# Optimization experiments

Measured on AMD Instinct MI355X. Metric: run time of the kernel, lower is better.

The kernel has to match this reference:

```python
import jax, jax.numpy as jnp
import numpy as np

N, C, B = 65536, 512, 4
H, P = 8, 256           # num_heads, patch_size
D = C // H              # head_dim = 64


def setup_inputs() -> dict:
    key = jax.random.key(0)
    k0, k1, k2 = jax.random.split(key, 3)
    x = jax.random.normal(k0, (N, C), dtype=jnp.float32)
    # sorted batch ids, equal-sized scenes (each divisible by patch_size)
    batch = (jnp.arange(N) // (N // B)).astype(jnp.int32)
    w_qkv = jax.random.normal(k1, (C, 3 * C), dtype=jnp.float32) * (C ** -0.5)
    b_qkv = jnp.zeros((3 * C,), dtype=jnp.float32)
    w_proj = jax.random.normal(k2, (C, C), dtype=jnp.float32) * (C ** -0.5)
    b_proj = jnp.zeros((C,), dtype=jnp.float32)
    return {"x": x, "batch": batch, "w_qkv": w_qkv, "b_qkv": b_qkv,
            "w_proj": w_proj, "b_proj": b_proj}


def reference(x, batch, w_qkv, b_qkv, w_proj, b_proj):
    # batch is sorted with per-scene counts divisible by P, so the original
    # per-batch mask/pad loop is exactly a global reshape into patches.
    n = x.shape[0]
    scale = D ** -0.5
    qkv = (x @ w_qkv + b_qkv).reshape(n, 3, H, D)
    q, k, v = qkv[:, 0], qkv[:, 1], qkv[:, 2]          # (N, H, D)
    q = q.reshape(-1, P, H, D)                          # (nP, P, H, D)
    k = k.reshape(-1, P, H, D)
    v = v.reshape(-1, P, H, D)
    attn = jnp.einsum('pihd,pjhd->phij', q, k) * scale  # (nP, H, P, P)
    attn = jax.nn.softmax(attn, axis=-1)
    out = jnp.einsum('phij,pjhd->pihd', attn, v)        # (nP, P, H, D)
    out = out.reshape(n, C)
    return out @ w_proj + b_proj
```

## Files before the change

### kernel.cpp

```cpp
#include <hip/hip_runtime.h>
#include <hip/hip_bf16.h>
#include <cstdint>

typedef __attribute__((ext_vector_type(8))) short bf16x8;
typedef __attribute__((ext_vector_type(4))) float f32x4;
typedef unsigned short u16;
typedef unsigned int u32;

#define MFMA16(a, b, c) __builtin_amdgcn_mfma_f32_16x16x32_bf16(a, b, c, 0, 0, 0)

__device__ __forceinline__ u16 f2bf(float f) {
  u32 u = __builtin_bit_cast(u32, f);
  u32 r = (u + 0x7fffu + ((u >> 16) & 1u)) >> 16;
  return (u16)r;
}

__device__ __forceinline__ void gload_lds16(const u16* g, u16* l) {
#if __has_builtin(__builtin_amdgcn_global_load_lds)
  __builtin_amdgcn_global_load_lds(
      (const __attribute__((address_space(1))) u32*)(const void*)g,
      (__attribute__((address_space(3))) u32*)(void*)l, 16, 0, 0);
#else
  *(uint4*)l = *(const uint4*)g;
#endif
}


__global__ __launch_bounds__(256) void cvt_x_kernel(const float* __restrict__ in,
                                                    u16* __restrict__ out, int n4) {
  const int stride = gridDim.x * blockDim.x;
  for (int i = blockIdx.x * blockDim.x + threadIdx.x; i < n4; i += stride) {
    float4 v = ((const float4*)in)[i];
    ushort4 o;
    o.x = f2bf(v.x); o.y = f2bf(v.y); o.z = f2bf(v.z); o.w = f2bf(v.w);
    ((ushort4*)out)[i] = o;
  }
}

__global__ __launch_bounds__(256) void transpose_kernel(const float* __restrict__ in,
                                                        u16* __restrict__ out,
                                                        int rows, int cols) {
  int idx = blockIdx.x * 256 + threadIdx.x;
  if (idx < rows * cols) {
    int c = idx / rows, r = idx - c * rows;
    out[idx] = f2bf(in[(size_t)r * cols + c]);
  }
}


template <bool OUT_BF16>
__global__ __launch_bounds__(256) void gemm_bt(const u16* __restrict__ A,
                                               const u16* __restrict__ Bt,
                                               const float* __restrict__ bias,
                                               void* __restrict__ Cout, int Ncols) {
  constexpr int K = 512;
  const int tm = blockIdx.x, tn = blockIdx.y;
  const int t = threadIdx.x;
  const int lane = t & 63, w = t >> 6;
  const int wr = w >> 1, wc = w & 1;
  const int fr = lane & 15, fq = lane >> 4;

  __shared__ __align__(16) u16 Als[128 * 64];
  __shared__ __align__(16) u16 Bls[128 * 64];

  f32x4 acc[4][4] = {};

  const u16* Ab = A + (size_t)tm * 128 * K;
  const u16* Bb = Bt + (size_t)tn * 128 * K;
  const int srow = t >> 3;
  const int scol = (t & 7) * 8;

  for (int ks = 0; ks < K; ks += 64) {
#pragma unroll
    for (int c = 0; c < 4; ++c) {
      gload_lds16(Ab + (size_t)(c * 32 + srow) * K + ks + scol, Als + c * 2048 + t * 8);
      gload_lds16(Bb + (size_t)(c * 32 + srow) * K + ks + scol, Bls + c * 2048 + t * 8);
    }
    __syncthreads();
#pragma unroll
    for (int kk = 0; kk < 2; ++kk) {
      bf16x8 af[4], bfr[4];
#pragma unroll
      for (int mt = 0; mt < 4; ++mt)
        af[mt] = *(const bf16x8*)(Als + (wr * 64 + mt * 16 + fr) * 64 + kk * 32 + fq * 8);
#pragma unroll
      for (int nt = 0; nt < 4; ++nt)
        bfr[nt] = *(const bf16x8*)(Bls + (wc * 64 + nt * 16 + fr) * 64 + kk * 32 + fq * 8);
#pragma unroll
      for (int mt = 0; mt < 4; ++mt)
#pragma unroll
        for (int nt = 0; nt < 4; ++nt)
          acc[mt][nt] = MFMA16(af[mt], bfr[nt], acc[mt][nt]);
    }
    __syncthreads();
  }

#pragma unroll
  for (int nt = 0; nt < 4; ++nt) {
    const int col = tn * 128 + wc * 64 + nt * 16 + fr;
    const float bv = bias[col];
#pragma unroll
    for (int mt = 0; mt < 4; ++mt) {
#pragma unroll
      for (int r = 0; r < 4; ++r) {
        const int row = tm * 128 + wr * 64 + mt * 16 + fq * 4 + r;
        float v = acc[mt][nt][r] + bv;
        if (OUT_BF16)
          ((u16*)Cout)[(size_t)row * Ncols + col] = f2bf(v);
        else
          ((float*)Cout)[(size_t)row * Ncols + col] = v;
      }
    }
  }
}


__global__ __launch_bounds__(512) void attn_kernel(const u16* __restrict__ qkv,
                                                   u16* __restrict__ out) {
  const int p = blockIdx.x, h = blockIdx.y;
  const int t = threadIdx.x, lane = t & 63, w = t >> 6;
  const int fr = lane & 15, fq = lane >> 4;

  __shared__ __align__(16) u16 Kls[256][72];
  __shared__ __align__(16) u16 Vt[64][264];
  __shared__ __align__(16) u16 Pls[8][32][72];

  const u16* base = qkv + (size_t)p * 256 * 1536 + h * 64;

#pragma unroll
  for (int it = 0; it < 4; ++it) {
    int chunk = it * 512 + t;
    int row = chunk >> 3, c8 = (chunk & 7) * 8;
    *(uint4*)&Kls[row][c8] = *(const uint4*)(base + (size_t)row * 1536 + 512 + c8);
  }
  {
    int token = t & 255, dh = (t >> 8) * 32;
    const u16* vs = base + (size_t)token * 1536 + 1024 + dh;
    uint4 b0 = *(const uint4*)(vs);
    uint4 b1 = *(const uint4*)(vs + 8);
    uint4 b2 = *(const uint4*)(vs + 16);
    uint4 b3 = *(const uint4*)(vs + 24);
    u16 tmp[32];
    *(uint4*)&tmp[0] = b0; *(uint4*)&tmp[8] = b1;
    *(uint4*)&tmp[16] = b2; *(uint4*)&tmp[24] = b3;
#pragma unroll
    for (int dd = 0; dd < 32; ++dd) Vt[dh + dd][token] = tmp[dd];
  }
  bf16x8 qf[2][2];
#pragma unroll
  for (int mt = 0; mt < 2; ++mt)
#pragma unroll
    for (int kk = 0; kk < 2; ++kk)
      qf[mt][kk] = *(const bf16x8*)(base + (size_t)(w * 32 + mt * 16 + fr) * 1536 + kk * 32 + fq * 8);
  __syncthreads();

  f32x4 Oc[2][4] = {};
  float mrow[2][4], lrow[2][4];
#pragma unroll
  for (int mt = 0; mt < 2; ++mt)
#pragma unroll
    for (int r = 0; r < 4; ++r) { mrow[mt][r] = -1e30f; lrow[mt][r] = 0.f; }

  for (int jb = 0; jb < 4; ++jb) {
    f32x4 S[2][4] = {};
#pragma unroll
    for (int kk = 0; kk < 2; ++kk) {
      bf16x8 kb[4];
#pragma unroll
      for (int jt = 0; jt < 4; ++jt)
        kb[jt] = *(const bf16x8*)&Kls[jb * 64 + jt * 16 + fr][kk * 32 + fq * 8];
#pragma unroll
      for (int mt = 0; mt < 2; ++mt)
#pragma unroll
        for (int jt = 0; jt < 4; ++jt)
          S[mt][jt] = MFMA16(qf[mt][kk], kb[jt], S[mt][jt]);
    }
#pragma unroll
    for (int mt = 0; mt < 2; ++mt) {
#pragma unroll
      for (int r = 0; r < 4; ++r) {
        float s0 = S[mt][0][r] * 0.125f, s1 = S[mt][1][r] * 0.125f;
        float s2 = S[mt][2][r] * 0.125f, s3 = S[mt][3][r] * 0.125f;
        float mx = fmaxf(fmaxf(s0, s1), fmaxf(s2, s3));
#pragma unroll
        for (int d = 1; d < 16; d <<= 1) mx = fmaxf(mx, __shfl_xor(mx, d, 64));
        float mnew = fmaxf(mrow[mt][r], mx);
        float alpha = __expf(mrow[mt][r] - mnew);
        mrow[mt][r] = mnew;
        float e0 = __expf(s0 - mnew), e1 = __expf(s1 - mnew);
        float e2 = __expf(s2 - mnew), e3 = __expf(s3 - mnew);
        S[mt][0][r] = e0; S[mt][1][r] = e1; S[mt][2][r] = e2; S[mt][3][r] = e3;
        float rs = e0 + e1 + e2 + e3;
#pragma unroll
        for (int d = 1; d < 16; d <<= 1) rs += __shfl_xor(rs, d, 64);
        lrow[mt][r] = lrow[mt][r] * alpha + rs;
#pragma unroll
        for (int dt = 0; dt < 4; ++dt) Oc[mt][dt][r] *= alpha;
      }
    }
#pragma unroll
    for (int mt = 0; mt < 2; ++mt)
#pragma unroll
      for (int jt = 0; jt < 4; ++jt)
#pragma unroll
        for (int r = 0; r < 4; ++r)
          Pls[w][mt * 16 + fq * 4 + r][jt * 16 + fr] = f2bf(S[mt][jt][r]);
    __syncthreads();
#pragma unroll
    for (int kk = 0; kk < 2; ++kk) {
      bf16x8 pa[2], vb[4];
#pragma unroll
      for (int mt = 0; mt < 2; ++mt)
        pa[mt] = *(const bf16x8*)&Pls[w][mt * 16 + fr][kk * 32 + fq * 8];
#pragma unroll
      for (int dt = 0; dt < 4; ++dt)
        vb[dt] = *(const bf16x8*)&Vt[dt * 16 + fr][jb * 64 + kk * 32 + fq * 8];
#pragma unroll
      for (int mt = 0; mt < 2; ++mt)
#pragma unroll
        for (int dt = 0; dt < 4; ++dt)
          Oc[mt][dt] = MFMA16(pa[mt], vb[dt], Oc[mt][dt]);
    }
  }
#pragma unroll
  for (int mt = 0; mt < 2; ++mt) {
#pragma unroll
    for (int r = 0; r < 4; ++r) {
      const float inv = 1.0f / lrow[mt][r];
      const int token = p * 256 + w * 32 + mt * 16 + fq * 4 + r;
#pragma unroll
      for (int dt = 0; dt < 4; ++dt)
        out[(size_t)token * 512 + h * 64 + dt * 16 + fr] = f2bf(Oc[mt][dt][r] * inv);
    }
  }
}


extern "C" void kernel_launch(void* const* d_in, const int* in_sizes, int n_in,
                              void* d_out, int out_size, void* d_ws, size_t ws_size,
                              hipStream_t stream) {
  const float* x      = (const float*)d_in[0];
  const float* w_qkv  = (const float*)d_in[2];
  const float* b_qkv  = (const float*)d_in[3];
  const float* w_proj = (const float*)d_in[4];
  const float* b_proj = (const float*)d_in[5];

  char* ws = (char*)d_ws;
  u16* xa     = (u16*)ws;
  u16* wqkvT  = (u16*)(ws + 67108864);
  u16* wprojT = (u16*)(ws + 68681728);
  u16* qkv    = (u16*)(ws + 69206016);
  u16* attn   = xa;

  cvt_x_kernel<<<2048, 256, 0, stream>>>(x, xa, 65536 * 512 / 4);
  transpose_kernel<<<(512 * 1536 + 255) / 256, 256, 0, stream>>>(w_qkv, wqkvT, 512, 1536);
  transpose_kernel<<<(512 * 512 + 255) / 256, 256, 0, stream>>>(w_proj, wprojT, 512, 512);

  gemm_bt<true><<<dim3(512, 12), 256, 0, stream>>>(xa, wqkvT, b_qkv, qkv, 1536);
  attn_kernel<<<dim3(256, 8), 512, 0, stream>>>(qkv, attn);
  gemm_bt<false><<<dim3(512, 4), 256, 0, stream>>>(attn, wprojT, b_proj, d_out, 512);
}
```

Baseline: 637.1 us.

## Replace GEMMs with 256x256-tile, 8-wave, double-buffered pipelined kernel

Both projection GEMMs now use a 256x256 tile per workgroup with 8 waves and double-buffered LDS. Global-to-LDS loads are interleaved with MFMA phases under explicit waitcnt and barrier control. LDS reads use an XOR swizzle to avoid bank conflicts, the workgroup order is remapped for better L2 locality, and MFMA phases raise wave priority. The aim is to hide memory latency and raise data reuse and MFMA utilisation, at the cost of higher register and LDS pressure and a fragile hand-written schedule.

```diff
diff --git a/kernel.cpp b/kernel.cpp
--- a/kernel.cpp
+++ b/kernel.cpp
@@ -16,13 +16,9 @@
 }
 
 __device__ __forceinline__ void gload_lds16(const u16* g, u16* l) {
-#if __has_builtin(__builtin_amdgcn_global_load_lds)
   __builtin_amdgcn_global_load_lds(
       (const __attribute__((address_space(1))) u32*)(const void*)g,
       (__attribute__((address_space(3))) u32*)(void*)l, 16, 0, 0);
-#else
-  *(uint4*)l = *(const uint4*)g;
-#endif
 }
 
 
@@ -48,62 +44,122 @@
 }
 
 
-template <bool OUT_BF16>
-__global__ __launch_bounds__(256) void gemm_bt(const u16* __restrict__ A,
-                                               const u16* __restrict__ Bt,
-                                               const float* __restrict__ bias,
-                                               void* __restrict__ Cout, int Ncols) {
+template <bool OUT_BF16, int NTN>
+__global__ __launch_bounds__(512, 2) void gemm8(const u16* __restrict__ A,
+                                                const u16* __restrict__ Bt,
+                                                const float* __restrict__ bias,
+                                                void* __restrict__ Cout, int Ncols) {
   constexpr int K = 512;
-  const int tm = blockIdx.x, tn = blockIdx.y;
-  const int t = threadIdx.x;
-  const int lane = t & 63, w = t >> 6;
-  const int wr = w >> 1, wc = w & 1;
+  const int nwg = gridDim.x;
+  const int q8 = nwg >> 3;
+  const int L = (blockIdx.x & 7) * q8 + (blockIdx.x >> 3);
+  const int tm = L / NTN, tn = L % NTN;
+
+  const int t = threadIdx.x, lane = t & 63, w = t >> 6;
+  const int wr = w >> 2, wc = w & 3;
   const int fr = lane & 15, fq = lane >> 4;
 
-  __shared__ __align__(16) u16 Als[128 * 64];
-  __shared__ __align__(16) u16 Bls[128 * 64];
-
-  f32x4 acc[4][4] = {};
-
-  const u16* Ab = A + (size_t)tm * 128 * K;
-  const u16* Bb = Bt + (size_t)tn * 128 * K;
-  const int srow = t >> 3;
-  const int scol = (t & 7) * 8;
-
-  for (int ks = 0; ks < K; ks += 64) {
-#pragma unroll
-    for (int c = 0; c < 4; ++c) {
-      gload_lds16(Ab + (size_t)(c * 32 + srow) * K + ks + scol, Als + c * 2048 + t * 8);
-      gload_lds16(Bb + (size_t)(c * 32 + srow) * K + ks + scol, Bls + c * 2048 + t * 8);
-    }
-    __syncthreads();
-#pragma unroll
-    for (int kk = 0; kk < 2; ++kk) {
-      bf16x8 af[4], bfr[4];
-#pragma unroll
-      for (int mt = 0; mt < 4; ++mt)
-        af[mt] = *(const bf16x8*)(Als + (wr * 64 + mt * 16 + fr) * 64 + kk * 32 + fq * 8);
-#pragma unroll
-      for (int nt = 0; nt < 4; ++nt)
-        bfr[nt] = *(const bf16x8*)(Bls + (wc * 64 + nt * 16 + fr) * 64 + kk * 32 + fq * 8);
-#pragma unroll
-      for (int mt = 0; mt < 4; ++mt)
-#pragma unroll
-        for (int nt = 0; nt < 4; ++nt)
-          acc[mt][nt] = MFMA16(af[mt], bfr[nt], acc[mt][nt]);
-    }
-    __syncthreads();
-  }
+  __shared__ __align__(16) u16 lds[2][2][2][8192];
+
+  const u16* Ab = A + (size_t)tm * 256 * K;
+  const u16* Bb = Bt + (size_t)tn * 256 * K;
+
+  int srow[2], scol[2];
+#pragma unroll
+  for (int i = 0; i < 2; ++i) {
+    const int cidx = t + i * 512;
+    const int rr = cidx >> 7, cc = (cidx >> 6) & 1, r16 = (cidx >> 2) & 15, qq = cidx & 3;
+    const int c8 = qq ^ ((r16 >> 3) << 1);
+    srow[i] = rr * 16 + r16;
+    scol[i] = cc * 32 + c8 * 8;
+  }
+
+  f32x4 acc[8][4] = {};
+  bf16x8 areg[4][2];
+  bf16x8 breg[4][2];
+
+  const int swz = (fq * 16) ^ ((fr & 8) << 2);
+
+#define STAGE(SB, SOP, SH, STK)                                                  \
+  {                                                                              \
+    const u16* gb_ = (SOP == 0) ? Ab : Bb;                                       \
+    u16* lb_ = &lds[SB][SOP][SH][0];                                             \
+    _Pragma("unroll") for (int i_ = 0; i_ < 2; ++i_) {                           \
+      gload_lds16(gb_ + (size_t)(SH * 128 + srow[i_]) * K + (STK) * 64 + scol[i_],\
+                  lb_ + (t + i_ * 512) * 8);                                     \
+    }                                                                            \
+  }
+
+#define LDA(RB, MH)                                                              \
+  {                                                                              \
+    const char* ab_ = (const char*)&lds[RB][0][wr][0];                           \
+    _Pragma("unroll") for (int m_ = 0; m_ < 4; ++m_)                             \
+      _Pragma("unroll") for (int kk_ = 0; kk_ < 2; ++kk_)                        \
+        areg[m_][kk_] = *(const bf16x8*)(ab_ + ((MH) * 4 + m_) * 2048 +          \
+                                         kk_ * 1024 + fr * 64 + swz);            \
+  }
+
+#define LDB(RB, NH)                                                              \
+  {                                                                              \
+    const char* bb_ = (const char*)&lds[RB][1][wc >> 1][0];                      \
+    _Pragma("unroll") for (int n_ = 0; n_ < 2; ++n_)                             \
+      _Pragma("unroll") for (int kk_ = 0; kk_ < 2; ++kk_)                        \
+        breg[(NH) * 2 + n_][kk_] = *(const bf16x8*)(bb_ +                        \
+            ((wc & 1) * 4 + (NH) * 2 + n_) * 2048 + kk_ * 1024 + fr * 64 + swz); \
+  }
+
+#define MMA(MH, NH)                                                              \
+  {                                                                              \
+    __builtin_amdgcn_s_setprio(1);                                               \
+    _Pragma("unroll") for (int m_ = 0; m_ < 4; ++m_)                             \
+      _Pragma("unroll") for (int n_ = 0; n_ < 2; ++n_)                           \
+        _Pragma("unroll") for (int kk_ = 0; kk_ < 2; ++kk_)                      \
+          acc[(MH) * 4 + m_][(NH) * 2 + n_] =                                    \
+              MFMA16(areg[m_][kk_], breg[(NH) * 2 + n_][kk_],                    \
+                     acc[(MH) * 4 + m_][(NH) * 2 + n_]);                         \
+    __builtin_amdgcn_s_setprio(0);                                               \
+  }
+
+#define BAR() __builtin_amdgcn_s_barrier()
+#define WLGKM() asm volatile("s_waitcnt lgkmcnt(0)" ::: "memory")
+#define WV4() asm volatile("s_waitcnt vmcnt(4)" ::: "memory")
+#define WV0() asm volatile("s_waitcnt vmcnt(0)" ::: "memory")
+
+  STAGE(0, 1, 0, 0) STAGE(0, 1, 1, 0) STAGE(0, 0, 0, 0) STAGE(0, 0, 1, 0)
+  STAGE(1, 1, 0, 1) STAGE(1, 1, 1, 1)
+  WV4();
+  BAR();
+
+#pragma unroll 1
+  for (int s = 0; s < 3; ++s) {
+    const int o1 = 2 * s + 1, e2 = 2 * s + 2, o3 = 2 * s + 3;
+    LDA(0, 0) LDB(0, 0) STAGE(1, 0, 0, o1) BAR(); WLGKM(); MMA(0, 0) BAR();
+    LDB(0, 1) STAGE(1, 0, 1, o1) BAR(); WLGKM(); MMA(0, 1) BAR();
+    LDA(0, 1) STAGE(0, 1, 0, e2) BAR(); WLGKM(); MMA(1, 0) BAR();
+    STAGE(0, 1, 1, e2) BAR(); MMA(1, 1) WV4(); BAR();
+    LDA(1, 0) LDB(1, 0) STAGE(0, 0, 0, e2) BAR(); WLGKM(); MMA(0, 0) BAR();
+    LDB(1, 1) STAGE(0, 0, 1, e2) BAR(); WLGKM(); MMA(0, 1) BAR();
+    LDA(1, 1) STAGE(1, 1, 0, o3) BAR(); WLGKM(); MMA(1, 0) BAR();
+    STAGE(1, 1, 1, o3) BAR(); MMA(1, 1) WV4(); BAR();
+  }
+  LDA(0, 0) LDB(0, 0) STAGE(1, 0, 0, 7) BAR(); WLGKM(); MMA(0, 0) BAR();
+  LDB(0, 1) STAGE(1, 0, 1, 7) BAR(); WLGKM(); MMA(0, 1) BAR();
+  LDA(0, 1) BAR(); WLGKM(); MMA(1, 0) BAR();
+  BAR(); MMA(1, 1) WV0(); BAR();
+  LDA(1, 0) LDB(1, 0) BAR(); WLGKM(); MMA(0, 0) BAR();
+  LDB(1, 1) BAR(); WLGKM(); MMA(0, 1) BAR();
+  LDA(1, 1) BAR(); WLGKM(); MMA(1, 0) BAR();
+  MMA(1, 1)
 
 #pragma unroll
   for (int nt = 0; nt < 4; ++nt) {
-    const int col = tn * 128 + wc * 64 + nt * 16 + fr;
+    const int col = tn * 256 + wc * 64 + nt * 16 + fr;
     const float bv = bias[col];
 #pragma unroll
-    for (int mt = 0; mt < 4; ++mt) {
+    for (int mt = 0; mt < 8; ++mt) {
 #pragma unroll
       for (int r = 0; r < 4; ++r) {
-        const int row = tm * 128 + wr * 64 + mt * 16 + fq * 4 + r;
+        const int row = tm * 256 + wr * 128 + mt * 16 + fq * 4 + r;
         float v = acc[mt][nt][r] + bv;
         if (OUT_BF16)
           ((u16*)Cout)[(size_t)row * Ncols + col] = f2bf(v);
@@ -112,6 +168,14 @@
       }
     }
   }
+#undef STAGE
+#undef LDA
+#undef LDB
+#undef MMA
+#undef BAR
+#undef WLGKM
+#undef WV4
+#undef WV0
 }
 
 
@@ -256,7 +320,7 @@
   transpose_kernel<<<(512 * 1536 + 255) / 256, 256, 0, stream>>>(w_qkv, wqkvT, 512, 1536);
   transpose_kernel<<<(512 * 512 + 255) / 256, 256, 0, stream>>>(w_proj, wprojT, 512, 512);
 
-  gemm_bt<true><<<dim3(512, 12), 256, 0, stream>>>(xa, wqkvT, b_qkv, qkv, 1536);
+  gemm8<true, 6><<<1536, 512, 0, stream>>>(xa, wqkvT, b_qkv, qkv, 1536);
   attn_kernel<<<dim3(256, 8), 512, 0, stream>>>(qkv, attn);
-  gemm_bt<false><<<dim3(512, 4), 256, 0, stream>>>(attn, wprojT, b_proj, d_out, 512);
-}
+  gemm8<false, 2><<<512, 512, 0, stream>>>(attn, wprojT, b_proj, d_out, 512);
+}
```

New measurement: 590.7 us. 1.08x faster.
